# Kernel optimization log

Hardware: AMD Instinct MI355X
Metric: run time of the kernel (lower is better)

Reference implementation:

```python
import jax, jax.numpy as jnp
import numpy as np

BATCH = 2048
DIMS = [256, 256, 256, 128]  # input, hidden, hidden, output
N_ATOMS = 4  # identity, sin, tanh, square


def setup_inputs() -> dict:
    key = jax.random.key(0)
    ks = jax.random.split(key, 8)
    inp = {"x": jax.random.normal(ks[0], (BATCH, DIMS[0]), dtype=jnp.float32)}
    for li in range(3):
        out_d, in_d = DIMS[li + 1], DIMS[li]
        inp[f"W{li}"] = jax.random.normal(ks[1 + li], (out_d, in_d), dtype=jnp.float32) * 0.1
        inp[f"b{li}"] = jnp.zeros((out_d,), dtype=jnp.float32)
        inp[f"f_idx{li}"] = jax.random.randint(ks[4 + li], (out_d, in_d), 0, N_ATOMS, dtype=jnp.int32)
    return inp


def _w_eff(W, idx):
    # per-element atom nonlinearity selected by idx: [identity, sin, tanh, square]
    atoms = jnp.stack([W, jnp.sin(W), jnp.tanh(W), W * W], axis=0)  # [A, out, in]
    return jnp.take_along_axis(atoms, idx[None].astype(jnp.int32), axis=0)[0]


def reference(x, W0, b0, W1, b1, W2, b2, f_idx0, f_idx1, f_idx2):
    layers = [(W0, b0, f_idx0), (W1, b1, f_idx1), (W2, b2, f_idx2)]
    h = x
    n = len(layers)
    for li, (W, b, idx) in enumerate(layers):
        We = _w_eff(W, idx)                       # [out, in]
        z = h[:, None, :] * We[None, :, :]        # [batch, out, in]
        gz = z if li == n - 1 else jnp.tanh(z)    # g_fixed='tanh' on hidden layers
        h = gz.sum(axis=-1) + b[None, :]          # [batch, out]
    return h
```

## Files before the change

### kernel.cpp

```cpp
#include <hip/hip_runtime.h>
#include <math.h>


typedef float v2f __attribute__((ext_vector_type(2)));

#define SC   2.885390081777927f
#define INV  (1.0f / 2.885390081777927f)
#define INV2PI 0.15915494309189535f
#define HS_CLAMP 32.0f
#define C8   0.00390625f

__device__ __forceinline__ float fast_rcp(float x)  { return __builtin_amdgcn_rcpf(x); }
__device__ __forceinline__ float fast_exp2(float x) { return __builtin_amdgcn_exp2f(x); }
__device__ __forceinline__ v2f pk2(float a, float b) { v2f r; r.x = a; r.y = b; return r; }

__device__ __forceinline__ v2f pk_add(v2f a, v2f b) {
    v2f d; asm("v_pk_add_f32 %0, %1, %2" : "=v"(d) : "v"(a), "v"(b)); return d;
}
__device__ __forceinline__ v2f pk_mul(v2f a, v2f b) {
    v2f d; asm("v_pk_mul_f32 %0, %1, %2" : "=v"(d) : "v"(a), "v"(b)); return d;
}
__device__ __forceinline__ v2f pk_fma(v2f a, v2f b, v2f c) {
    v2f d; asm("v_pk_fma_f32 %0, %1, %2, %3" : "=v"(d) : "v"(a), "v"(b), "v"(c)); return d;
}
__device__ __forceinline__ v2f pk_fma_lo(v2f a, v2f s, v2f c) {
    v2f d; asm("v_pk_fma_f32 %0, %1, %2, %3 op_sel_hi:[1,0,1]"
               : "=v"(d) : "v"(a), "v"(s), "v"(c)); return d;
}
__device__ __forceinline__ v2f pk_fma_hi(v2f a, v2f s, v2f c) {
    v2f d; asm("v_pk_fma_f32 %0, %1, %2, %3 op_sel:[0,1,0] op_sel_hi:[1,1,1]"
               : "=v"(d) : "v"(a), "v"(s), "v"(c)); return d;
}
__device__ __forceinline__ v2f pk_exp(v2f t) {
    v2f e; e.x = fast_exp2(t.x); e.y = fast_exp2(t.y); return e;
}
__device__ __forceinline__ v2f lo2(float4 w) { return pk2(w.x, w.y); }
__device__ __forceinline__ v2f hi2(float4 w) { return pk2(w.z, w.w); }

__global__ void weff_kernel(const float* __restrict__ W0, const int* __restrict__ I0,
                            const float* __restrict__ W1, const int* __restrict__ I1,
                            const float* __restrict__ W2, const int* __restrict__ I2,
                            float* __restrict__ ws) {
    int tid = blockIdx.x * blockDim.x + threadIdx.x;
    const float* W; const int* I; float* out; int outd; int e;
    if (tid < 65536)        { W = W0; I = I0; out = ws;          outd = 256; e = tid; }
    else if (tid < 131072)  { W = W1; I = I1; out = ws + 65536;  outd = 256; e = tid - 65536; }
    else if (tid < 163840)  { W = W2; I = I2; out = ws + 131072; outd = 128; e = tid - 131072; }
    else return;
    int o = e >> 8;
    int i = e & 255;
    float w = W[e];
    int idx = I[e];
    float sn = __builtin_amdgcn_sinf(w * INV2PI);
    float th = 1.0f - 2.0f * fast_rcp(fast_exp2(w * SC) + 1.0f);
    float sq = w * w;
    float v = (idx == 1) ? sn : (idx == 2) ? th : (idx == 3) ? sq : w;
    out[(i >> 2) * (outd * 4) + o * 4 + (i & 3)] = v;
}

struct ND { v2f n, d; };
__device__ __forceinline__ ND tree4(float4 pa, float4 pb, float4 w, v2f m8, v2f c8) {
    v2f h0 = pk2(pa.x, pa.y), h1 = pk2(pa.z, pa.w);
    v2f h2 = pk2(pb.x, pb.y), h3 = pk2(pb.z, pb.w);
    v2f wxy = lo2(w), wzw = hi2(w);
    v2f B0 = pk_add(pk_exp(pk_fma_lo(h0, wxy, m8)), c8);
    v2f B1 = pk_add(pk_exp(pk_fma_hi(h1, wxy, m8)), c8);
    v2f B2 = pk_add(pk_exp(pk_fma_lo(h2, wzw, m8)), c8);
    v2f B3 = pk_add(pk_exp(pk_fma_hi(h3, wzw, m8)), c8);
    v2f S1 = pk_add(B0, B1), P1 = pk_mul(B0, B1);
    v2f S2 = pk_add(B2, B3), P2 = pk_mul(B2, B3);
    ND r;
    r.n = pk_fma(S2, P1, pk_mul(S1, P2));
    r.d = pk_mul(P1, P2);
    return r;
}

__device__ __forceinline__ v2f sig8_acc(ND a, ND b, v2f acc) {
    v2f num = pk_fma(b.n, a.d, pk_mul(a.n, b.d));
    v2f den = pk_mul(a.d, b.d);
    v2f rd;  rd.x = fast_rcp(den.x); rd.y = fast_rcp(den.y);
    return pk_fma(num, rd, acc);
}

__global__ __launch_bounds__(512, 4) void mlp_kernel(
    const float* __restrict__ x,  const float* __restrict__ b0,
    const float* __restrict__ b1, const float* __restrict__ b2,
    const float* __restrict__ ws, float* __restrict__ out) {
    const float4* We0 = (const float4*)ws;
    const float4* We1 = (const float4*)(ws + 65536);
    const float4* We2 = (const float4*)(ws + 131072);

    __shared__ __align__(16) v2f hA0[256];
    __shared__ __align__(16) v2f hA1[256];
    __shared__ __align__(16) v2f hB0[256];
    __shared__ __align__(16) v2f hB1[256];
    __shared__ __align__(16) v2f partA[512];
    __shared__ __align__(16) v2f partB[512];

    const int t = threadIdx.x;
    const int g = t >> 8;
    const int o = t & 255;
    const int row0 = blockIdx.x * 4;

    const v2f m8 = pk2(-8.0f, -8.0f);
    const v2f c8 = pk2(C8, C8);

    {
        float xv = x[(row0 + g) * 256 + o] * SC;
        xv = fminf(fmaxf(xv, -HS_CLAMP), HS_CLAMP);
        ((float*)&hA0[o])[g] = xv;
        float xw = x[(row0 + 2 + g) * 256 + o] * SC;
        xw = fminf(fmaxf(xw, -HS_CLAMP), HS_CLAMP);
        ((float*)&hA1[o])[g] = xw;
    }
    __syncthreads();

    {
        const float bias = b0[o];
        v2f acc0 = pk2(0.f, 0.f), acc1 = pk2(0.f, 0.f);
#pragma unroll 2
        for (int icc = 0; icc < 32; icc += 2) {
            int ic = g * 32 + icc;
            float4 w0 = We0[ic * 256 + o];
            float4 w1 = We0[(ic + 1) * 256 + o];
            const float4* hp0 = (const float4*)(hA0 + ic * 4);
            const float4* hp1 = (const float4*)(hA1 + ic * 4);
            ND r0 = tree4(hp0[0], hp0[1], w0, m8, c8);
            ND r1 = tree4(hp0[2], hp0[3], w1, m8, c8);
            acc0 = sig8_acc(r0, r1, acc0);
            ND r2 = tree4(hp1[0], hp1[1], w0, m8, c8);
            ND r3 = tree4(hp1[2], hp1[3], w1, m8, c8);
            acc1 = sig8_acc(r2, r3, acc1);
        }
        partA[g * 256 + o] = acc0;
        partB[g * 256 + o] = acc1;
        __syncthreads();
        float s0 = ((const float*)(partA + o))[g] + ((const float*)(partA + 256 + o))[g];
        float h0 = (256.0f - 0.0078125f * s0 + bias) * SC;
        h0 = fminf(fmaxf(h0, -HS_CLAMP), HS_CLAMP);
        ((float*)&hB0[o])[g] = h0;
        float s1 = ((const float*)(partB + o))[g] + ((const float*)(partB + 256 + o))[g];
        float h1 = (256.0f - 0.0078125f * s1 + bias) * SC;
        h1 = fminf(fmaxf(h1, -HS_CLAMP), HS_CLAMP);
        ((float*)&hB1[o])[g] = h1;
        __syncthreads();
    }

    {
        const float bias = b1[o];
        v2f acc0 = pk2(0.f, 0.f), acc1 = pk2(0.f, 0.f);
#pragma unroll 2
        for (int icc = 0; icc < 32; icc += 2) {
            int ic = g * 32 + icc;
            float4 w0 = We1[ic * 256 + o];
            float4 w1 = We1[(ic + 1) * 256 + o];
            const float4* hp0 = (const float4*)(hB0 + ic * 4);
            const float4* hp1 = (const float4*)(hB1 + ic * 4);
            ND r0 = tree4(hp0[0], hp0[1], w0, m8, c8);
            ND r1 = tree4(hp0[2], hp0[3], w1, m8, c8);
            acc0 = sig8_acc(r0, r1, acc0);
            ND r2 = tree4(hp1[0], hp1[1], w0, m8, c8);
            ND r3 = tree4(hp1[2], hp1[3], w1, m8, c8);
            acc1 = sig8_acc(r2, r3, acc1);
        }
        partA[g * 256 + o] = acc0;
        partB[g * 256 + o] = acc1;
        __syncthreads();
        float s0 = ((const float*)(partA + o))[g] + ((const float*)(partA + 256 + o))[g];
        float h0 = (256.0f - 0.0078125f * s0 + bias) * SC;
        h0 = fminf(fmaxf(h0, -HS_CLAMP), HS_CLAMP);
        ((float*)&hA0[o])[g] = h0;
        float s1 = ((const float*)(partB + o))[g] + ((const float*)(partB + 256 + o))[g];
        float h1 = (256.0f - 0.0078125f * s1 + bias) * SC;
        h1 = fminf(fmaxf(h1, -HS_CLAMP), HS_CLAMP);
        ((float*)&hB1[o])[g] = h1;
        __syncthreads();
    }

    {
        const int o2 = t & 127;
        const int q  = t >> 7;
        v2f acc0 = pk2(0.f, 0.f), acc1 = pk2(0.f, 0.f);
#pragma unroll 4
        for (int icc = 0; icc < 16; icc++) {
            int ic = q * 16 + icc;
            float4 w = We2[ic * 128 + o2];
            const float4* hp0 = (const float4*)(hA0 + ic * 4);
            const float4* hp1 = (const float4*)(hB1 + ic * 4);
            float4 pa = hp0[0], pb = hp0[1];
            float4 qa = hp1[0], qb = hp1[1];
            v2f wxy = lo2(w), wzw = hi2(w);
            acc0 = pk_fma_lo(pk2(pa.x, pa.y), wxy, acc0);
            acc0 = pk_fma_hi(pk2(pa.z, pa.w), wxy, acc0);
            acc0 = pk_fma_lo(pk2(pb.x, pb.y), wzw, acc0);
            acc0 = pk_fma_hi(pk2(pb.z, pb.w), wzw, acc0);
            acc1 = pk_fma_lo(pk2(qa.x, qa.y), wxy, acc1);
            acc1 = pk_fma_hi(pk2(qa.z, qa.w), wxy, acc1);
            acc1 = pk_fma_lo(pk2(qb.x, qb.y), wzw, acc1);
            acc1 = pk_fma_hi(pk2(qb.z, qb.w), wzw, acc1);
        }
        partA[q * 128 + o2] = acc0;
        partB[q * 128 + o2] = acc1;
        __syncthreads();
        const int r  = t >> 7;
        const int oo = t & 127;
        const v2f* prt = (r & 2) ? partB : partA;
        const int  ln  = r & 1;
        float s = ((const float*)(prt + oo))[ln]
                + ((const float*)(prt + 128 + oo))[ln]
                + ((const float*)(prt + 256 + oo))[ln]
                + ((const float*)(prt + 384 + oo))[ln];
        out[(row0 + r) * 128 + oo] = s * INV + b2[oo];
    }
}

extern "C" void kernel_launch(void* const* d_in, const int* in_sizes, int n_in,
                              void* d_out, int out_size, void* d_ws, size_t ws_size,
                              hipStream_t stream) {
    const float* x  = (const float*)d_in[0];
    const float* W0 = (const float*)d_in[1];
    const float* b0 = (const float*)d_in[2];
    const int*   I0 = (const int*)  d_in[3];
    const float* W1 = (const float*)d_in[4];
    const float* b1 = (const float*)d_in[5];
    const int*   I1 = (const int*)  d_in[6];
    const float* W2 = (const float*)d_in[7];
    const float* b2 = (const float*)d_in[8];
    const int*   I2 = (const int*)  d_in[9];
    float* ws  = (float*)d_ws;
    float* out = (float*)d_out;

    weff_kernel<<<640, 256, 0, stream>>>(W0, I0, W1, I1, W2, I2, ws);
    mlp_kernel<<<512, 512, 0, stream>>>(x, b0, b1, b2, ws, out);
}
```

Measured before the change: 113.2 us.

## Double block size to 1024 threads and split input-dim reduction four ways

Grows the block to 1024 threads while keeping 4 rows per block, so each layer's input-dimension reduction is split across 4 (and 8 for the last layer) thread groups instead of 2 (and 4). Partial-sum buffers are doubled and the final reduction sums more partials, with each thread handling one row/output pair. The aim is more parallelism per block and shorter per-thread loops, at the cost of more shared-memory partials, extra reduction work and a lower launch-bounds occupancy hint.

New measurement: 117.8 us. 4.1% more time.

```diff
diff --git a/kernel.cpp b/kernel.cpp
--- a/kernel.cpp
+++ b/kernel.cpp
@@ -82,7 +82,7 @@
     return pk_fma(num, rd, acc);
 }
 
-__global__ __launch_bounds__(512, 4) void mlp_kernel(
+__global__ __launch_bounds__(1024) void mlp_kernel(
     const float* __restrict__ x,  const float* __restrict__ b0,
     const float* __restrict__ b1, const float* __restrict__ b2,
     const float* __restrict__ ws, float* __restrict__ out) {
@@ -94,8 +94,8 @@
     __shared__ __align__(16) v2f hA1[256];
     __shared__ __align__(16) v2f hB0[256];
     __shared__ __align__(16) v2f hB1[256];
-    __shared__ __align__(16) v2f partA[512];
-    __shared__ __align__(16) v2f partB[512];
+    __shared__ __align__(16) v2f partA[1024];
+    __shared__ __align__(16) v2f partB[1024];
 
     const int t = threadIdx.x;
     const int g = t >> 8;
@@ -106,12 +106,11 @@
     const v2f c8 = pk2(C8, C8);
 
     {
-        float xv = x[(row0 + g) * 256 + o] * SC;
+        const int rs = t >> 8;
+        float xv = x[(row0 + rs) * 256 + o] * SC;
         xv = fminf(fmaxf(xv, -HS_CLAMP), HS_CLAMP);
-        ((float*)&hA0[o])[g] = xv;
-        float xw = x[(row0 + 2 + g) * 256 + o] * SC;
-        xw = fminf(fmaxf(xw, -HS_CLAMP), HS_CLAMP);
-        ((float*)&hA1[o])[g] = xw;
+        v2f* H = (rs & 2) ? hA1 : hA0;
+        ((float*)(H + o))[rs & 1] = xv;
     }
     __syncthreads();
 
@@ -119,8 +118,8 @@
         const float bias = b0[o];
         v2f acc0 = pk2(0.f, 0.f), acc1 = pk2(0.f, 0.f);
 #pragma unroll 2
-        for (int icc = 0; icc < 32; icc += 2) {
-            int ic = g * 32 + icc;
+        for (int icc = 0; icc < 16; icc += 2) {
+            int ic = g * 16 + icc;
             float4 w0 = We0[ic * 256 + o];
             float4 w1 = We0[(ic + 1) * 256 + o];
             const float4* hp0 = (const float4*)(hA0 + ic * 4);
@@ -135,14 +134,16 @@
         partA[g * 256 + o] = acc0;
         partB[g * 256 + o] = acc1;
         __syncthreads();
-        float s0 = ((const float*)(partA + o))[g] + ((const float*)(partA + 256 + o))[g];
-        float h0 = (256.0f - 0.0078125f * s0 + bias) * SC;
-        h0 = fminf(fmaxf(h0, -HS_CLAMP), HS_CLAMP);
-        ((float*)&hB0[o])[g] = h0;
-        float s1 = ((const float*)(partB + o))[g] + ((const float*)(partB + 256 + o))[g];
-        float h1 = (256.0f - 0.0078125f * s1 + bias) * SC;
-        h1 = fminf(fmaxf(h1, -HS_CLAMP), HS_CLAMP);
-        ((float*)&hB1[o])[g] = h1;
+        const v2f* P = (g & 2) ? partB : partA;
+        const int  ln = g & 1;
+        float s = ((const float*)(P + o))[ln]
+                + ((const float*)(P + 256 + o))[ln]
+                + ((const float*)(P + 512 + o))[ln]
+                + ((const float*)(P + 768 + o))[ln];
+        float h = (256.0f - 0.0078125f * s + bias) * SC;
+        h = fminf(fmaxf(h, -HS_CLAMP), HS_CLAMP);
+        v2f* H = (g & 2) ? hB1 : hB0;
+        ((float*)(H + o))[ln] = h;
         __syncthreads();
     }
 
@@ -150,8 +151,8 @@
         const float bias = b1[o];
         v2f acc0 = pk2(0.f, 0.f), acc1 = pk2(0.f, 0.f);
 #pragma unroll 2
-        for (int icc = 0; icc < 32; icc += 2) {
-            int ic = g * 32 + icc;
+        for (int icc = 0; icc < 16; icc += 2) {
+            int ic = g * 16 + icc;
             float4 w0 = We1[ic * 256 + o];
             float4 w1 = We1[(ic + 1) * 256 + o];
             const float4* hp0 = (const float4*)(hB0 + ic * 4);
@@ -166,14 +167,16 @@
         partA[g * 256 + o] = acc0;
         partB[g * 256 + o] = acc1;
         __syncthreads();
-        float s0 = ((const float*)(partA + o))[g] + ((const float*)(partA + 256 + o))[g];
-        float h0 = (256.0f - 0.0078125f * s0 + bias) * SC;
-        h0 = fminf(fmaxf(h0, -HS_CLAMP), HS_CLAMP);
-        ((float*)&hA0[o])[g] = h0;
-        float s1 = ((const float*)(partB + o))[g] + ((const float*)(partB + 256 + o))[g];
-        float h1 = (256.0f - 0.0078125f * s1 + bias) * SC;
-        h1 = fminf(fmaxf(h1, -HS_CLAMP), HS_CLAMP);
-        ((float*)&hB1[o])[g] = h1;
+        const v2f* P = (g & 2) ? partB : partA;
+        const int  ln = g & 1;
+        float s = ((const float*)(P + o))[ln]
+                + ((const float*)(P + 256 + o))[ln]
+                + ((const float*)(P + 512 + o))[ln]
+                + ((const float*)(P + 768 + o))[ln];
+        float h = (256.0f - 0.0078125f * s + bias) * SC;
+        h = fminf(fmaxf(h, -HS_CLAMP), HS_CLAMP);
+        v2f* H = (g & 2) ? hA1 : hA0;
+        ((float*)(H + o))[ln] = h;
         __syncthreads();
     }
 
@@ -182,11 +185,11 @@
         const int q  = t >> 7;
         v2f acc0 = pk2(0.f, 0.f), acc1 = pk2(0.f, 0.f);
 #pragma unroll 4
-        for (int icc = 0; icc < 16; icc++) {
-            int ic = q * 16 + icc;
+        for (int icc = 0; icc < 8; icc++) {
+            int ic = q * 8 + icc;
             float4 w = We2[ic * 128 + o2];
             const float4* hp0 = (const float4*)(hA0 + ic * 4);
-            const float4* hp1 = (const float4*)(hB1 + ic * 4);
+            const float4* hp1 = (const float4*)(hA1 + ic * 4);
             float4 pa = hp0[0], pb = hp0[1];
             float4 qa = hp1[0], qb = hp1[1];
             v2f wxy = lo2(w), wzw = hi2(w);
@@ -202,15 +205,17 @@
         partA[q * 128 + o2] = acc0;
         partB[q * 128 + o2] = acc1;
         __syncthreads();
-        const int r  = t >> 7;
-        const int oo = t & 127;
-        const v2f* prt = (r & 2) ? partB : partA;
-        const int  ln  = r & 1;
-        float s = ((const float*)(prt + oo))[ln]
-                + ((const float*)(prt + 128 + oo))[ln]
-                + ((const float*)(prt + 256 + oo))[ln]
-                + ((const float*)(prt + 384 + oo))[ln];
-        out[(row0 + r) * 128 + oo] = s * INV + b2[oo];
+        if (t < 512) {
+            const int r  = t >> 7;
+            const int oo = t & 127;
+            const v2f* prt = (r & 2) ? partB : partA;
+            const int  ln  = r & 1;
+            float s = 0.f;
+#pragma unroll
+            for (int q2 = 0; q2 < 8; q2++)
+                s += ((const float*)(prt + q2 * 128 + oo))[ln];
+            out[(row0 + r) * 128 + oo] = s * INV + b2[oo];
+        }
     }
 }
 
@@ -231,5 +236,5 @@
     float* out = (float*)d_out;
 
     weff_kernel<<<640, 256, 0, stream>>>(W0, I0, W1, I1, W2, I2, ws);
-    mlp_kernel<<<512, 512, 0, stream>>>(x, b0, b1, b2, ws, out);
-}
+    mlp_kernel<<<512, 1024, 0, stream>>>(x, b0, b1, b2, ws, out);
+}
```
